# Optimization experiments

Measured on AMD Instinct MI355X. Metric: run time of the kernel, lower is better.

Reference implementation:

```python
import jax, jax.numpy as jnp
import numpy as np

B = 4096
ED = 128          # EMBEDDING_DIM
HD = 64           # HIDDEN_DIM
LH = 128          # LSTM_HIDDEN_DIM
IN_DIM = ED * (12 + 48 + 1)  # 7808
N_ABILITY, N_MOVE = 300, 900


def setup_inputs() -> dict:
    key = jax.random.key(0)
    ks = jax.random.split(key, 16)
    s = lambda k, shape, scale=0.05: (jax.random.normal(k, shape, dtype=jnp.float32) * scale)
    return {
        "ability_ids": jax.random.randint(ks[0], (B, 12), 0, N_ABILITY),
        "move_ids": jax.random.randint(ks[1], (B, 48), 0, N_MOVE),
        "numerical": s(ks[2], (B, 84), 1.0),
        "mask": (jax.random.uniform(ks[3], (B, 9)) > 0.3).astype(jnp.float32),
        "h0": jnp.zeros((B, LH), jnp.float32),
        "c0": jnp.zeros((B, LH), jnp.float32),
        "ability_emb": s(ks[4], (N_ABILITY, ED), 1.0),
        "move_emb": s(ks[5], (N_MOVE, ED), 1.0),
        "num_W": s(ks[6], (ED, 84)),
        "num_b": s(ks[7], (ED,)),
        "Wih": s(ks[8], (4 * LH, IN_DIM), 0.01),
        "Whh": s(ks[9], (4 * LH, LH)),
        "bih": s(ks[10], (4 * LH,)),
        "bhh": s(ks[11], (4 * LH,)),
        "W1": s(ks[12], (HD, LH)),
        "b1": s(ks[13], (HD,)),
        "W2": s(ks[14], (ED, HD)),
        "b2": s(ks[15], (ED,)),
        "Wa": s(jax.random.fold_in(key, 100), (9, ED)),
        "ba": s(jax.random.fold_in(key, 101), (9,)),
    }


def reference(ability_ids, move_ids, numerical, mask, h0, c0,
              ability_emb, move_emb, num_W, num_b,
              Wih, Whh, bih, bhh, W1, b1, W2, b2, Wa, ba):
    # Gather + concat: [B, 12*ED] + [B, 48*ED] + [B, ED] -> [B, 7808]
    ab = ability_emb[ability_ids].reshape(ability_ids.shape[0], 12 * ED)
    mv = move_emb[move_ids].reshape(move_ids.shape[0], 48 * ED)
    num = numerical @ num_W.T + num_b
    x = jnp.concatenate([ab, mv, num], axis=-1)

    # Single-timestep LSTM (torch gate order: i, f, g, o)
    gates = x @ Wih.T + bih + h0 @ Whh.T + bhh
    i, f, g, o = jnp.split(gates, 4, axis=-1)
    i, f, o = jax.nn.sigmoid(i), jax.nn.sigmoid(f), jax.nn.sigmoid(o)
    g = jnp.tanh(g)
    c1 = f * c0 + i * g
    h1 = o * jnp.tanh(c1)

    # MLP head + action logits
    feat = jax.nn.relu(h1 @ W1.T + b1) @ W2.T + b2
    probs = jax.nn.softmax(feat @ Wa.T + ba, axis=-1)

    # Masked renormalization; fall back to unmasked probs when mask kills everything
    masked = probs * mask
    ssum = masked.sum(-1, keepdims=True)
    out = jnp.where(ssum > 0, masked / jnp.where(ssum > 0, ssum, 1.0), probs)
    return out, h1, c1
```

## Files before the change

### kernel.cpp

```cpp
#include <hip/hip_runtime.h>
#include <hip/hip_bf16.h>
#include <stdint.h>
#include <stddef.h>

typedef __bf16 bf16;
typedef __bf16 bf16x8 __attribute__((ext_vector_type(8)));
typedef float f32x4 __attribute__((ext_vector_type(4)));

#define BATCH 4096
#define KIH 7808
#define KTOT 7936
#define NG 512
#define LH 128
#define HD 64
#define ED 128
#define SPLITK 4

#define OFF_WCAT 0u
#define OFF_GPART 8126464u
#define OFF_XT   41680896u
#define OFF_AB   43778048u
#define OFF_MV   43854848u
#define OFF_ADDR 44085248u

#define O_H1 (BATCH * 9)
#define O_C1 (BATCH * 9 + BATCH * LH)

typedef const __attribute__((address_space(1))) uint32_t* gas_ptr;
typedef __attribute__((address_space(3))) uint32_t* las_ptr;

__device__ __forceinline__ void async16(const void* g, void* l) {
    __builtin_amdgcn_global_load_lds((gas_ptr)g, (las_ptr)l, 16, 0, 0);
}

__global__ void prep(const int* __restrict__ ab_ids,
                     const int* __restrict__ mv_ids,
                     const float* __restrict__ numerical,
                     const float* __restrict__ h0,
                     const float* __restrict__ numW,
                     const float* __restrict__ numb,
                     const float* __restrict__ Wih,
                     const float* __restrict__ Whh,
                     const float* __restrict__ ab_emb,
                     const float* __restrict__ mv_emb,
                     uint8_t* __restrict__ ws) {
    const int bid = blockIdx.x;
    const int t = threadIdx.x;

    if (bid < BATCH) {
        bf16* xtail = (bf16*)(ws + OFF_XT);
        uint32_t* addrs = (uint32_t*)(ws + OFF_ADDR);
        const int b = bid;

        __shared__ int ids[60];
        __shared__ float numr[84];
        if (t < 60) ids[t] = (t < 12) ? ab_ids[b * 12 + t] : mv_ids[b * 48 + (t - 12)];
        if (t >= 128 && t < 128 + 84) numr[t - 128] = numerical[(size_t)b * 84 + (t - 128)];
        __syncthreads();

        if (t < 128) {
            float acc = numb[t];
#pragma unroll 4
            for (int k = 0; k < 84; ++k)
                acc += numr[k] * numW[t * 84 + k];
            xtail[(size_t)b * 256 + t] = (bf16)acc;
        } else {
            const int tt = t - 128;
            xtail[(size_t)b * 256 + 128 + tt] = (bf16)h0[(size_t)b * LH + tt];
        }

        if (t < 64) {
            uint32_t off;
            if (t < 12) off = OFF_AB + (uint32_t)ids[t] * 256u;
            else if (t < 60) off = OFF_MV + (uint32_t)ids[t] * 256u;
            else if (t == 60) off = OFF_XT + (uint32_t)b * 512u;
            else if (t == 61) off = OFF_XT + (uint32_t)b * 512u + 256u;
            else off = OFF_XT;
            addrs[(size_t)b * 64 + t] = off;
        }
    } else if (bid < BATCH + 512) {
        bf16* Wcat = (bf16*)(ws + OFF_WCAT);
        const int n = bid - BATCH;
        const float* src_ih = Wih + (size_t)n * KIH;
        const float* src_hh = Whh + (size_t)n * LH;
        bf16* dst = Wcat + (size_t)n * KTOT;
        for (int k4 = t; k4 < KTOT / 4; k4 += 256) {
            const int k = k4 * 4;
            const float4 v = (k < KIH) ? *(const float4*)(src_ih + k)
                                       : *(const float4*)(src_hh + (k - KIH));
            bf16 o0 = (bf16)v.x, o1 = (bf16)v.y, o2 = (bf16)v.z, o3 = (bf16)v.w;
            dst[k] = o0; dst[k + 1] = o1; dst[k + 2] = o2; dst[k + 3] = o3;
        }
    } else {
        bf16* ab8 = (bf16*)(ws + OFF_AB);
        bf16* mv8 = (bf16*)(ws + OFF_MV);
        const int i = (bid - BATCH - 512) * 256 + t;
        if (i < 300 * 128) ab8[i] = (bf16)ab_emb[i];
        else if (i < 1200 * 128) mv8[i - 300 * 128] = (bf16)mv_emb[i - 300 * 128];
    }
}

__global__ __launch_bounds__(512, 2) void gemm_gates(
    const uint8_t* __restrict__ wsbase,
    const bf16* __restrict__ Wcat,
    const uint32_t* __restrict__ addrs,
    float* __restrict__ gpart) {
    __shared__ bf16 As[2][256 * 64];
    __shared__ bf16 Bs[2][128 * 64];
    __shared__ uint32_t adr[16][256];

    const int tid = threadIdx.x;
    const int w = tid >> 6;
    const int lane = tid & 63;
    const int bm = blockIdx.x;
    const int bn = blockIdx.y;
    const int bz = blockIdx.z;
    const int kt_beg = bz * 31;
    const int kt_end = kt_beg + 31;

    const int s0 = kt_beg >> 1;
    const int ns = ((kt_end - 1) >> 1) - s0 + 1;
    for (int i = tid; i < ns * 256; i += 512) {
        adr[i >> 8][i & 255] =
            addrs[(size_t)(bm * 256 + (i & 255)) * 64 + s0 + (i >> 8)];
    }

    const int r_l = lane >> 3;
    const int sc16 = ((lane & 7) ^ r_l) * 16;

    f32x4 acc[4][4];
#pragma unroll
    for (int i = 0; i < 4; ++i)
#pragma unroll
        for (int j = 0; j < 4; ++j)
#pragma unroll
            for (int r = 0; r < 4; ++r) acc[i][j][r] = 0.f;

    const int wm = w & 3, wn = w >> 2;
    const int m0 = wm * 64;
    const int n0 = wn * 64;

    __syncthreads();

    auto stage = [&](int kt, int pb) {
        const int k0 = kt * 64;
        const int sl = (kt >> 1) - s0;
        const int hb = (kt & 1) * 128;
#pragma unroll
        for (int j = 0; j < 4; ++j) {
            const int g = w * 4 + j;
            const int row = g * 8 + r_l;
            const uint8_t* gsrc = wsbase + adr[sl][row] + hb + sc16;
            async16(gsrc, (void*)&As[pb][(g * 64 + lane) * 8]);
        }
#pragma unroll
        for (int j = 0; j < 2; ++j) {
            const int g = w * 2 + j;
            const int row = g * 8 + r_l;
            const bf16* gsrc = Wcat + (size_t)(bn * 128 + row) * KTOT + k0 + (sc16 >> 1);
            async16(gsrc, (void*)&Bs[pb][(g * 64 + lane) * 8]);
        }
    };

    stage(kt_beg, 0);

    for (int kt = kt_beg; kt < kt_end; ++kt) {
        const int pb = (kt - kt_beg) & 1;
        __syncthreads();
        if (kt + 1 < kt_end) stage(kt + 1, pb ^ 1);

        const bf16* Ab = &As[pb][0];
        const bf16* Bb = &Bs[pb][0];
#pragma unroll
        for (int ks = 0; ks < 2; ++ks) {
            bf16x8 af[4], bfr[4];
            const int kk8 = ks * 4 + (lane >> 4);
#pragma unroll
            for (int t = 0; t < 4; ++t) {
                const int m = m0 + t * 16 + (lane & 15);
                af[t] = *(const bf16x8*)&Ab[m * 64 + ((kk8 ^ (m & 7)) * 8)];
                const int n = n0 + t * 16 + (lane & 15);
                bfr[t] = *(const bf16x8*)&Bb[n * 64 + ((kk8 ^ (n & 7)) * 8)];
            }
#pragma unroll
            for (int ti = 0; ti < 4; ++ti)
#pragma unroll
                for (int tj = 0; tj < 4; ++tj)
                    acc[ti][tj] = __builtin_amdgcn_mfma_f32_16x16x32_bf16(
                        af[ti], bfr[tj], acc[ti][tj], 0, 0, 0);
        }
    }

    float* gdst = gpart + (size_t)bz * BATCH * NG;
    const int mlo = (lane >> 4) * 4;
    const int nlo = lane & 15;
#pragma unroll
    for (int ti = 0; ti < 4; ++ti)
#pragma unroll
        for (int tj = 0; tj < 4; ++tj) {
            const int mg = bm * 256 + m0 + ti * 16 + mlo;
            const int ng = bn * 128 + n0 + tj * 16 + nlo;
            float* dst = gdst + (size_t)mg * NG + ng;
#pragma unroll
            for (int r = 0; r < 4; ++r)
                dst[(size_t)r * NG] = acc[ti][tj][r];
        }
}

__global__ __launch_bounds__(128, 3) void tail(
    const float* __restrict__ gpart, const float* __restrict__ bih,
    const float* __restrict__ bhh, const float* __restrict__ c0,
    const float* __restrict__ mask,
    const float* __restrict__ W1, const float* __restrict__ b1,
    const float* __restrict__ W2, const float* __restrict__ b2,
    const float* __restrict__ Wa, const float* __restrict__ ba,
    float* __restrict__ out) {
    __shared__ bf16 W1f[8192];
    __shared__ bf16 W2f[8192];
    __shared__ bf16 Waf[2048];
    __shared__ bf16 h1s[16 * 128];
    __shared__ bf16 uS[16 * 64];
    __shared__ bf16 fS[16 * 128];
    __shared__ float b1s[64];
    __shared__ float b2s[128];
    __shared__ float bas[16];

    const int tid = threadIdx.x;
    const int b0 = blockIdx.x * 16;

    for (int e = tid; e < 8192; e += 128) {
        const int j = e & 7, ln = (e >> 3) & 63, fid = e >> 9;
        const int kt = fid & 3, nt = fid >> 2;
        const int n = nt * 16 + (ln & 15);
        const int k = kt * 32 + (ln >> 4) * 8 + j;
        W1f[e] = (bf16)W1[n * 128 + k];
    }
    for (int e = tid; e < 8192; e += 128) {
        const int j = e & 7, ln = (e >> 3) & 63, fid = e >> 9;
        const int kt = fid & 1, nt = fid >> 1;
        const int n = nt * 16 + (ln & 15);
        const int k = kt * 32 + (ln >> 4) * 8 + j;
        W2f[e] = (bf16)W2[n * 64 + k];
    }
    for (int e = tid; e < 2048; e += 128) {
        const int j = e & 7, ln = (e >> 3) & 63, kt = e >> 9;
        const int n = ln & 15;
        const int k = kt * 32 + (ln >> 4) * 8 + j;
        Waf[e] = (n < 9) ? (bf16)Wa[n * 128 + k] : (bf16)0.f;
    }
    if (tid < 64) b1s[tid] = b1[tid];
    if (tid < 16) bas[tid] = (tid < 9) ? ba[tid] : 0.f;
    if (tid < 128) b2s[tid] = b2[tid];

#pragma unroll
    for (int i = 0; i < 16; ++i) {
        const int p = tid + 128 * i;
        const int uu = p & 127;
        const int r = p >> 7;
        const int b = b0 + r;
        float gv[4];
#pragma unroll
        for (int q = 0; q < 4; ++q)
            gv[q] = bih[q * 128 + uu] + bhh[q * 128 + uu];
#pragma unroll
        for (int z = 0; z < SPLITK; ++z) {
            const float* gz = gpart + ((size_t)z * BATCH + b) * NG + uu;
#pragma unroll
            for (int q = 0; q < 4; ++q) gv[q] += gz[q * 128];
        }
        const float iv = 1.f / (1.f + __expf(-gv[0]));
        const float fv = 1.f / (1.f + __expf(-gv[1]));
        const float gg = tanhf(gv[2]);
        const float ov = 1.f / (1.f + __expf(-gv[3]));
        const float c1 = fv * c0[(size_t)b * LH + uu] + iv * gg;
        const float h1 = ov * tanhf(c1);
        out[O_H1 + (size_t)b * LH + uu] = h1;
        out[O_C1 + (size_t)b * LH + uu] = c1;
        h1s[r * 128 + uu] = (bf16)h1;
    }
    __syncthreads();

    const int wv = tid >> 6, lane = tid & 63;
    const int nl = lane & 15, kg = lane >> 4;

    bf16x8 ah[4];
#pragma unroll
    for (int kt = 0; kt < 4; ++kt)
        ah[kt] = *(const bf16x8*)&h1s[nl * 128 + kt * 32 + kg * 8];

#pragma unroll
    for (int t2 = 0; t2 < 2; ++t2) {
        const int nt = wv * 2 + t2;
        f32x4 a = {0.f, 0.f, 0.f, 0.f};
#pragma unroll
        for (int kt = 0; kt < 4; ++kt)
            a = __builtin_amdgcn_mfma_f32_16x16x32_bf16(
                ah[kt], *(const bf16x8*)&W1f[((nt * 4 + kt) * 64 + lane) * 8], a, 0, 0, 0);
        const int n = nt * 16 + nl;
#pragma unroll
        for (int r = 0; r < 4; ++r)
            uS[(kg * 4 + r) * 64 + n] = (bf16)fmaxf(a[r] + b1s[n], 0.f);
    }
    __syncthreads();

    bf16x8 au[2];
#pragma unroll
    for (int kt = 0; kt < 2; ++kt)
        au[kt] = *(const bf16x8*)&uS[nl * 64 + kt * 32 + kg * 8];

#pragma unroll
    for (int t2 = 0; t2 < 4; ++t2) {
        const int nt = wv * 4 + t2;
        f32x4 a = {0.f, 0.f, 0.f, 0.f};
#pragma unroll
        for (int kt = 0; kt < 2; ++kt)
            a = __builtin_amdgcn_mfma_f32_16x16x32_bf16(
                au[kt], *(const bf16x8*)&W2f[((nt * 2 + kt) * 64 + lane) * 8], a, 0, 0, 0);
        const int n = nt * 16 + nl;
#pragma unroll
        for (int r = 0; r < 4; ++r)
            fS[(kg * 4 + r) * 128 + n] = (bf16)(a[r] + b2s[n]);
    }
    __syncthreads();

    if (wv == 0) {
        bf16x8 afr[4];
#pragma unroll
        for (int kt = 0; kt < 4; ++kt)
            afr[kt] = *(const bf16x8*)&fS[nl * 128 + kt * 32 + kg * 8];

        f32x4 lg4 = {0.f, 0.f, 0.f, 0.f};
#pragma unroll
        for (int kt = 0; kt < 4; ++kt)
            lg4 = __builtin_amdgcn_mfma_f32_16x16x32_bf16(
                afr[kt], *(const bf16x8*)&Waf[(kt * 64 + lane) * 8], lg4, 0, 0, 0);

#pragma unroll
        for (int r = 0; r < 4; ++r) {
            const int b = b0 + kg * 4 + r;
            float lg = (nl < 9) ? lg4[r] + bas[nl] : -1e30f;
            float mx = lg;
#pragma unroll
            for (int off = 1; off < 16; off <<= 1)
                mx = fmaxf(mx, __shfl_xor(mx, off, 64));
            const float e = (nl < 9) ? __expf(lg - mx) : 0.f;
            const float mv = (nl < 9) ? mask[(size_t)b * 9 + nl] : 0.f;
            float tot = e, ms = e * mv;
#pragma unroll
            for (int off = 1; off < 16; off <<= 1) {
                tot += __shfl_xor(tot, off, 64);
                ms += __shfl_xor(ms, off, 64);
            }
            if (nl < 9)
                out[(size_t)b * 9 + nl] = (ms > 0.f) ? e * mv / ms : e / tot;
        }
    }
}

extern "C" void kernel_launch(void* const* d_in, const int* in_sizes, int n_in,
                              void* d_out, int out_size, void* d_ws, size_t ws_size,
                              hipStream_t stream) {
    const int* ab_ids = (const int*)d_in[0];
    const int* mv_ids = (const int*)d_in[1];
    const float* numerical = (const float*)d_in[2];
    const float* mask = (const float*)d_in[3];
    const float* h0 = (const float*)d_in[4];
    const float* c0 = (const float*)d_in[5];
    const float* ab_emb = (const float*)d_in[6];
    const float* mv_emb = (const float*)d_in[7];
    const float* numW = (const float*)d_in[8];
    const float* numb = (const float*)d_in[9];
    const float* Wih = (const float*)d_in[10];
    const float* Whh = (const float*)d_in[11];
    const float* bih = (const float*)d_in[12];
    const float* bhh = (const float*)d_in[13];
    const float* W1 = (const float*)d_in[14];
    const float* b1 = (const float*)d_in[15];
    const float* W2 = (const float*)d_in[16];
    const float* b2 = (const float*)d_in[17];
    const float* Wa = (const float*)d_in[18];
    const float* ba = (const float*)d_in[19];
    float* out = (float*)d_out;

    uint8_t* ws = (uint8_t*)d_ws;
    bf16* Wcat = (bf16*)(ws + OFF_WCAT);
    float* gpart = (float*)(ws + OFF_GPART);
    uint32_t* addrs = (uint32_t*)(ws + OFF_ADDR);

    prep<<<BATCH + 512 + 600, 256, 0, stream>>>(
        ab_ids, mv_ids, numerical, h0, numW, numb, Wih, Whh, ab_emb, mv_emb, ws);
    gemm_gates<<<dim3(16, 4, SPLITK), 512, 0, stream>>>(ws, Wcat, addrs, gpart);
    tail<<<BATCH / 16, 128, 0, stream>>>(gpart, bih, bhh, c0, mask,
                                         W1, b1, W2, b2, Wa, ba, out);
}
```

Baseline: 195.3 us.

## Load GEMM fragments directly from global into registers, dropping LDS staging

The gates GEMM no longer stages A and B tiles through shared memory with async global-to-LDS copies. Each wave now loads its MFMA operand fragments straight from global memory into registers, double-buffered across two register banks. Tiles shrink to 256x64 per 256-thread block and the grid doubles in N, so more blocks run with fewer barriers. The cost is that operand reuse across waves now goes through L2/L1 instead of LDS, adding redundant global traffic and uncoalesced 16-byte gathers, plus more register pressure.

New measurement: 262.8 us. 34.6% more time.

```diff
diff --git a/kernel.cpp b/kernel.cpp
--- a/kernel.cpp
+++ b/kernel.cpp
@@ -25,13 +25,6 @@
 
 #define O_H1 (BATCH * 9)
 #define O_C1 (BATCH * 9 + BATCH * LH)
-
-typedef const __attribute__((address_space(1))) uint32_t* gas_ptr;
-typedef __attribute__((address_space(3))) uint32_t* las_ptr;
-
-__device__ __forceinline__ void async16(const void* g, void* l) {
-    __builtin_amdgcn_global_load_lds((gas_ptr)g, (las_ptr)l, 16, 0, 0);
-}
 
 __global__ void prep(const int* __restrict__ ab_ids,
                      const int* __restrict__ mv_ids,
@@ -100,14 +93,12 @@
     }
 }
 
-__global__ __launch_bounds__(512, 2) void gemm_gates(
+__global__ __launch_bounds__(256, 2) void gemm_gates(
     const uint8_t* __restrict__ wsbase,
     const bf16* __restrict__ Wcat,
     const uint32_t* __restrict__ addrs,
     float* __restrict__ gpart) {
-    __shared__ bf16 As[2][256 * 64];
-    __shared__ bf16 Bs[2][128 * 64];
-    __shared__ uint32_t adr[16][256];
+    __shared__ uint32_t adr[17][256];
 
     const int tid = threadIdx.x;
     const int w = tid >> 6;
@@ -117,16 +108,21 @@
     const int bz = blockIdx.z;
     const int kt_beg = bz * 31;
     const int kt_end = kt_beg + 31;
-
     const int s0 = kt_beg >> 1;
     const int ns = ((kt_end - 1) >> 1) - s0 + 1;
-    for (int i = tid; i < ns * 256; i += 512) {
+
+    for (int i = tid; i < ns * 256; i += 256)
         adr[i >> 8][i & 255] =
             addrs[(size_t)(bm * 256 + (i & 255)) * 64 + s0 + (i >> 8)];
-    }
-
-    const int r_l = lane >> 3;
-    const int sc16 = ((lane & 7) ^ r_l) * 16;
+    __syncthreads();
+
+    const int nl = lane & 15;
+    const int kg = lane >> 4;
+
+    const bf16* pB[4];
+#pragma unroll
+    for (int t = 0; t < 4; ++t)
+        pB[t] = Wcat + (size_t)(bn * 64 + t * 16 + nl) * KTOT + kg * 8;
 
     f32x4 acc[4][4];
 #pragma unroll
@@ -136,70 +132,66 @@
 #pragma unroll
             for (int r = 0; r < 4; ++r) acc[i][j][r] = 0.f;
 
-    const int wm = w & 3, wn = w >> 2;
-    const int m0 = wm * 64;
-    const int n0 = wn * 64;
-
-    __syncthreads();
-
-    auto stage = [&](int kt, int pb) {
-        const int k0 = kt * 64;
+    uint32_t aofs[4];
+
+    auto refresh = [&](int kt) {
         const int sl = (kt >> 1) - s0;
+#pragma unroll
+        for (int t = 0; t < 4; ++t)
+            aofs[t] = adr[sl][w * 64 + t * 16 + nl];
+    };
+
+    auto loadbank = [&](int kt, bf16x8 (&af)[4][2], bf16x8 (&bfr)[4][2]) {
         const int hb = (kt & 1) * 128;
-#pragma unroll
-        for (int j = 0; j < 4; ++j) {
-            const int g = w * 4 + j;
-            const int row = g * 8 + r_l;
-            const uint8_t* gsrc = wsbase + adr[sl][row] + hb + sc16;
-            async16(gsrc, (void*)&As[pb][(g * 64 + lane) * 8]);
-        }
-#pragma unroll
-        for (int j = 0; j < 2; ++j) {
-            const int g = w * 2 + j;
-            const int row = g * 8 + r_l;
-            const bf16* gsrc = Wcat + (size_t)(bn * 128 + row) * KTOT + k0 + (sc16 >> 1);
-            async16(gsrc, (void*)&Bs[pb][(g * 64 + lane) * 8]);
+        const size_t bofs = (size_t)kt * 64;
+#pragma unroll
+        for (int t = 0; t < 4; ++t) {
+            const uint8_t* pa = wsbase + aofs[t] + hb + kg * 16;
+            af[t][0] = *(const bf16x8*)(pa);
+            af[t][1] = *(const bf16x8*)(pa + 64);
+            bfr[t][0] = *(const bf16x8*)(pB[t] + bofs);
+            bfr[t][1] = *(const bf16x8*)(pB[t] + bofs + 32);
         }
     };
 
-    stage(kt_beg, 0);
-
-    for (int kt = kt_beg; kt < kt_end; ++kt) {
-        const int pb = (kt - kt_beg) & 1;
-        __syncthreads();
-        if (kt + 1 < kt_end) stage(kt + 1, pb ^ 1);
-
-        const bf16* Ab = &As[pb][0];
-        const bf16* Bb = &Bs[pb][0];
-#pragma unroll
-        for (int ks = 0; ks < 2; ++ks) {
-            bf16x8 af[4], bfr[4];
-            const int kk8 = ks * 4 + (lane >> 4);
-#pragma unroll
-            for (int t = 0; t < 4; ++t) {
-                const int m = m0 + t * 16 + (lane & 15);
-                af[t] = *(const bf16x8*)&Ab[m * 64 + ((kk8 ^ (m & 7)) * 8)];
-                const int n = n0 + t * 16 + (lane & 15);
-                bfr[t] = *(const bf16x8*)&Bb[n * 64 + ((kk8 ^ (n & 7)) * 8)];
-            }
+    auto compute = [&](bf16x8 (&af)[4][2], bf16x8 (&bfr)[4][2]) {
+#pragma unroll
+        for (int ks = 0; ks < 2; ++ks)
 #pragma unroll
             for (int ti = 0; ti < 4; ++ti)
 #pragma unroll
                 for (int tj = 0; tj < 4; ++tj)
                     acc[ti][tj] = __builtin_amdgcn_mfma_f32_16x16x32_bf16(
-                        af[ti], bfr[tj], acc[ti][tj], 0, 0, 0);
-        }
-    }
+                        af[ti][ks], bfr[tj][ks], acc[ti][tj], 0, 0, 0);
+    };
+
+    bf16x8 a0[4][2], b0[4][2], a1[4][2], b1[4][2];
+
+    int kt = kt_beg;
+    refresh(kt);
+    loadbank(kt, a0, b0);
+#pragma unroll 1
+    for (int it = 0; it < 15; ++it) {
+        const int k1 = kt + 1;
+        if ((k1 & 1) == 0) refresh(k1);
+        loadbank(k1, a1, b1);
+        compute(a0, b0);
+        const int k2 = kt + 2;
+        if ((k2 & 1) == 0) refresh(k2);
+        loadbank(k2, a0, b0);
+        compute(a1, b1);
+        kt += 2;
+    }
+    compute(a0, b0);
 
     float* gdst = gpart + (size_t)bz * BATCH * NG;
-    const int mlo = (lane >> 4) * 4;
-    const int nlo = lane & 15;
+    const int mlo = kg * 4;
 #pragma unroll
     for (int ti = 0; ti < 4; ++ti)
 #pragma unroll
         for (int tj = 0; tj < 4; ++tj) {
-            const int mg = bm * 256 + m0 + ti * 16 + mlo;
-            const int ng = bn * 128 + n0 + tj * 16 + nlo;
+            const int mg = bm * 256 + w * 64 + ti * 16 + mlo;
+            const int ng = bn * 64 + tj * 16 + nl;
             float* dst = gdst + (size_t)mg * NG + ng;
 #pragma unroll
             for (int r = 0; r < 4; ++r)
@@ -389,7 +381,7 @@
 
     prep<<<BATCH + 512 + 600, 256, 0, stream>>>(
         ab_ids, mv_ids, numerical, h0, numW, numb, Wih, Whh, ab_emb, mv_emb, ws);
-    gemm_gates<<<dim3(16, 4, SPLITK), 512, 0, stream>>>(ws, Wcat, addrs, gpart);
+    gemm_gates<<<dim3(16, 8, SPLITK), 256, 0, stream>>>(ws, Wcat, addrs, gpart);
     tail<<<BATCH / 16, 128, 0, stream>>>(gpart, bih, bhh, c0, mask,
                                          W1, b1, W2, b2, Wa, ba, out);
 }
```
